# Kernel tuning notes

Hardware: AMD Instinct MI355X
Metric: run time of the kernel (lower is better)

Reference implementation:

```python
import jax, jax.numpy as jnp
import numpy as np

N, D, H1, H2 = 8192, 768, 512, 256


def _nig_head(x, W1, b1, W2, b2, Wh, bh):
    # Linear -> GELU -> (dropout=id) -> Linear -> GELU -> Linear head, then softplus transforms
    h = jax.nn.gelu(x @ W1 + b1, approximate=False)
    h = jax.nn.gelu(h @ W2 + b2, approximate=False)
    r = h @ Wh + bh  # [N, 4]
    mu = r[:, 0]
    v = jax.nn.softplus(r[:, 1]) + 1e-6
    a = jax.nn.softplus(r[:, 2]) + 1.0 + 1e-6
    b = jax.nn.softplus(r[:, 3]) + 1e-6
    return mu, v, a, b


def setup_inputs() -> dict:
    key = jax.random.key(0)
    ks = jax.random.split(key, 16)
    f32 = jnp.float32
    sd = 1.0 / np.sqrt(D)

    def lin(k, din, dout):
        kw, kb = jax.random.split(k)
        W = jax.random.normal(kw, (din, dout), f32) * (1.0 / np.sqrt(din))
        b = jax.random.normal(kb, (dout,), f32) * 0.01
        return W, b

    X = jax.random.normal(ks[0], (N, D), f32)
    Wq = jax.random.normal(ks[1], (D, D), f32) * sd
    Wk = jax.random.normal(ks[2], (D, D), f32) * sd
    Wg, bg = lin(ks[3], D, D)
    gam = jnp.array(1.0, f32)
    ih_W1, ih_b1 = lin(ks[4], D, H1)
    ih_W2, ih_b2 = lin(ks[5], H1, H2)
    ih_Wh, ih_bh = lin(ks[6], H2, 4)
    fh_W1, fh_b1 = lin(ks[7], D, H1)
    fh_W2, fh_b2 = lin(ks[8], H1, H2)
    fh_Wh, fh_bh = lin(ks[9], H2, 4)
    return {
        "X": X, "Wq": Wq, "Wk": Wk, "Wg": Wg, "bg": bg, "gam": gam,
        "ih_W1": ih_W1, "ih_b1": ih_b1, "ih_W2": ih_W2, "ih_b2": ih_b2,
        "ih_Wh": ih_Wh, "ih_bh": ih_bh,
        "fh_W1": fh_W1, "fh_b1": fh_b1, "fh_W2": fh_W2, "fh_b2": fh_b2,
        "fh_Wh": fh_Wh, "fh_bh": fh_bh,
    }


def reference(X, Wq, Wk, Wg, bg, gam,
              ih_W1, ih_b1, ih_W2, ih_b2, ih_Wh, ih_bh,
              fh_W1, fh_b1, fh_W2, fh_b2, fh_Wh, fh_bh):
    # initial NIG head -> epistemic uncertainty -> gate
    m0, v0, a0, b0 = _nig_head(X, ih_W1, ih_b1, ih_W2, ih_b2, ih_Wh, ih_bh)
    u0 = b0 / jnp.maximum(a0 - 1.0, 1e-8)
    G = 1.0 - gam * jax.nn.sigmoid(u0)  # [N]

    # dense attention adjacency
    scale = jnp.sqrt(jnp.asarray(D, X.dtype))
    Q = X @ Wq
    K = X @ Wk
    A = jax.nn.softmax(Q @ K.T / scale, axis=-1)  # [N, N]

    # uncertainty outer-product gate + row renormalization
    A_gated = A * G[None, :] * G[:, None]
    Dinv = 1.0 / jnp.maximum(A_gated.sum(-1, keepdims=True), 1e-8)

    # degree-normalized GCN aggregation + linear + GELU
    M = jax.nn.gelu((A_gated * Dinv) @ X @ Wg + bg, approximate=False)

    # final NIG head on residual
    mu, v, al, be = _nig_head(X + M, fh_W1, fh_b1, fh_W2, fh_b2, fh_Wh, fh_bh)
    return (m0, v0, a0, b0, mu, v, al, be)
```

## Files before the change

kernel.cpp:

```cpp
#include <hip/hip_runtime.h>
#include <hip/hip_bf16.h>
#include <hip/hip_fp8.h>
#include <math.h>
#include <stdint.h>
#include <stddef.h>


#define NT    8192
#define DD    768
#define DH1   512
#define DH2   256
#define SPAN  4096

typedef __attribute__((ext_vector_type(8))) short  short8;
typedef __attribute__((ext_vector_type(4))) float  f32x4;
typedef __attribute__((ext_vector_type(2))) long   longx2;

#define MFMA16(a, b, c) __builtin_amdgcn_mfma_f32_16x16x32_bf16((a), (b), (c), 0, 0, 0)
#define MFMAF8(a, b, c) __builtin_amdgcn_mfma_f32_16x16x32_fp8_fp8((a), (b), (c), 0, 0, 0)

__device__ __forceinline__ float bf2f(__hip_bfloat16 x) { return __bfloat162float(x); }
__device__ __forceinline__ __hip_bfloat16 f2bf(float x) { return __float2bfloat16(x); }
__device__ __forceinline__ uint8_t f2fp8(float x) { return __hip_fp8_e4m3(x).__x; }

__device__ __forceinline__ float gelu_f(float x) {
    return 0.5f * x * (1.0f + erff(x * 0.7071067811865476f));
}
__device__ __forceinline__ float softplus_f(float x) {
    return (x > 20.0f) ? x : log1pf(expf(x));
}

__device__ __forceinline__ void gload16(const void* g, void* l) {
    __builtin_amdgcn_global_load_lds(
        (const __attribute__((address_space(1))) void*)g,
        (__attribute__((address_space(3))) void*)l, 16, 0, 0);
}

template <int N>
__device__ __forceinline__ void wait_barrier() {
    asm volatile("s_waitcnt vmcnt(%0)\n\ts_barrier" :: "i"(N) : "memory");
}
__device__ __forceinline__ void plain_barrier() {
    asm volatile("s_barrier" ::: "memory");
}

__device__ __forceinline__ void xcd_remap(int& bx, int& by) {
    const int nbx = gridDim.x, nby = gridDim.y;
    if ((nby & 7) == 0) {
        const int lin = by * nbx + bx;
        const int x   = lin & 7;
        const int s   = lin >> 3;
        bx = s % nbx;
        by = x + 8 * (s / nbx);
    }
}

template <int EPI, bool SPLIT, int TM, int TN>
__global__ __launch_bounds__(256)
void gemm_bt(const __hip_bfloat16* __restrict__ Ahi, const __hip_bfloat16* __restrict__ Alo, int lda,
             const __hip_bfloat16* __restrict__ Bhi, const __hip_bfloat16* __restrict__ Blo, int ldb,
             __hip_bfloat16* __restrict__ obf_hi, __hip_bfloat16* __restrict__ obf_lo,
             uint8_t* __restrict__ of8, int ldc,
             const float* __restrict__ bias, int K)
{
    constexpr int NB  = SPLIT ? 2 : 1;
    constexpr int WRM = (TM == 128 && TN == 128) ? 2 : (TM == 128 ? 4 : 2);
    constexpr int WCN = 4 / WRM;
    constexpr int WTM = TM / WRM;
    constexpr int WTN = TN / WCN;
    constexpr int MI  = WTM / 16;
    constexpr int NI  = WTN / 16;
    constexpr int PA  = TM / 64;
    constexpr int PB  = TN / 64;
    constexpr int LPI = (PA + PB) * NB;

    __shared__ __align__(16) __hip_bfloat16 As[NB][2][TM * 32];
    __shared__ __align__(16) __hip_bfloat16 Bs[NB][2][TN * 32];

    const int tid  = threadIdx.x;
    const int wave = tid >> 6;
    const int lane = tid & 63;
    int bx = blockIdx.x, by = blockIdx.y;
    xcd_remap(bx, by);
    const int tm = by * TM;
    const int tn = bx * TN;

    const int srow  = tid >> 2;
    const int sgcol = ((tid & 3) ^ ((srow >> 1) & 3)) * 8;
    const int lofs  = srow * 32 + (tid & 3) * 8;

    size_t aoffs[PA], boffs[PB];
#pragma unroll
    for (int p = 0; p < PA; ++p) aoffs[p] = (size_t)(tm + p * 64 + srow) * lda + sgcol;
#pragma unroll
    for (int p = 0; p < PB; ++p) boffs[p] = (size_t)(tn + p * 64 + srow) * ldb + sgcol;

    auto stage = [&](int k0, int buf) {
#pragma unroll
        for (int p = 0; p < PA; ++p)
            gload16(Ahi + aoffs[p] + k0, &As[0][buf][p * 2048 + lofs]);
#pragma unroll
        for (int p = 0; p < PB; ++p)
            gload16(Bhi + boffs[p] + k0, &Bs[0][buf][p * 2048 + lofs]);
        if constexpr (SPLIT) {
#pragma unroll
            for (int p = 0; p < PA; ++p)
                gload16(Alo + aoffs[p] + k0, &As[1][buf][p * 2048 + lofs]);
#pragma unroll
            for (int p = 0; p < PB; ++p)
                gload16(Blo + boffs[p] + k0, &Bs[1][buf][p * 2048 + lofs]);
        }
    };

    f32x4 acc[MI][NI];
#pragma unroll
    for (int i = 0; i < MI; ++i)
#pragma unroll
        for (int j = 0; j < NI; ++j) {
            f32x4 z = {0.0f, 0.0f, 0.0f, 0.0f};
            acc[i][j] = z;
        }

    const int wm   = (wave / WCN) * WTM;
    const int wn   = (wave % WCN) * WTN;
    const int l16  = lane & 15;
    const int quad = lane >> 4;
    const int rchunk = (quad ^ ((l16 >> 1) & 3)) * 8;
    const int arow0  = (wm + l16) * 32 + rchunk;
    const int brow0  = (wn + l16) * 32 + rchunk;

    const int nIter = K >> 5;
    stage(0, 0);
    for (int k = 0; k < nIter; ++k) {
        const int cb = k & 1;
        if (k + 1 < nIter) {
            stage((k + 1) << 5, cb ^ 1);
            wait_barrier<LPI>();
        } else {
            wait_barrier<0>();
        }

        short8 ah[MI], bh[NI];
#pragma unroll
        for (int i = 0; i < MI; ++i) ah[i] = *(const short8*)&As[0][cb][arow0 + i * 512];
#pragma unroll
        for (int j = 0; j < NI; ++j) bh[j] = *(const short8*)&Bs[0][cb][brow0 + j * 512];
        if constexpr (SPLIT) {
            short8 al[MI], bl[NI];
#pragma unroll
            for (int i = 0; i < MI; ++i) al[i] = *(const short8*)&As[1][cb][arow0 + i * 512];
#pragma unroll
            for (int j = 0; j < NI; ++j) bl[j] = *(const short8*)&Bs[1][cb][brow0 + j * 512];
#pragma unroll
            for (int mi = 0; mi < MI; ++mi)
#pragma unroll
                for (int ni = 0; ni < NI; ++ni) {
                    acc[mi][ni] = MFMA16(ah[mi], bh[ni], acc[mi][ni]);
                    acc[mi][ni] = MFMA16(ah[mi], bl[ni], acc[mi][ni]);
                    acc[mi][ni] = MFMA16(al[mi], bh[ni], acc[mi][ni]);
                }
        } else {
#pragma unroll
            for (int mi = 0; mi < MI; ++mi)
#pragma unroll
                for (int ni = 0; ni < NI; ++ni)
                    acc[mi][ni] = MFMA16(ah[mi], bh[ni], acc[mi][ni]);
        }
        plain_barrier();
    }

    const int rbase = tm + wm + quad * 4;
    const int cbase = tn + wn + l16;

    if constexpr (EPI == 0) {
#pragma unroll
        for (int mi = 0; mi < MI; ++mi)
#pragma unroll
            for (int ni = 0; ni < NI; ++ni) {
                f32x4 v = acc[mi][ni];
                const int col = cbase + ni * 16;
#pragma unroll
                for (int r = 0; r < 4; ++r) {
                    size_t idx = (size_t)(rbase + mi * 16 + r) * ldc + col;
                    if (obf_hi) obf_hi[idx] = f2bf(v[r]);
                    if (of8)    of8[idx]    = f2fp8(v[r]);
                }
            }
    } else {
#pragma unroll
        for (int mi = 0; mi < MI; ++mi)
#pragma unroll
            for (int ni = 0; ni < NI; ++ni) {
                f32x4 v = acc[mi][ni];
                const int col = cbase + ni * 16;
                const float b = bias[col];
#pragma unroll
                for (int r = 0; r < 4; ++r) {
                    float g = gelu_f(v[r] + b);
                    __hip_bfloat16 h = f2bf(g);
                    size_t idx = (size_t)(rbase + mi * 16 + r) * ldc + col;
                    obf_hi[idx] = h;
                    if (obf_lo) obf_lo[idx] = f2bf(g - bf2f(h));
                }
            }
    }
}

template <int EPI, int TM, int TN>
__global__ __launch_bounds__(256)
void gemm_f8(const uint8_t* __restrict__ A, int lda,
             const uint8_t* __restrict__ B, int ldb,
             uint8_t* __restrict__ of8, int ldc,
             const float* __restrict__ Gv, float* __restrict__ Esum,
             float* __restrict__ Tsum,
             const float* __restrict__ Xf, const float* __restrict__ bg2,
             const float* __restrict__ Grow, const float* __restrict__ Erow,
             const float* __restrict__ Trow,
             __hip_bfloat16* __restrict__ Yout, int K)
{
    constexpr int WRM = (TM == 128 && TN == 128) ? 2 : (TM == 128 ? 4 : 2);
    constexpr int WCN = 4 / WRM;
    constexpr int WTM = TM / WRM;
    constexpr int WTN = TN / WCN;
    constexpr int MI  = WTM / 16;
    constexpr int NI  = WTN / 16;
    constexpr int PA  = TM / 64;
    constexpr int PB  = TN / 64;
    constexpr int LPI = PA + PB;

    __shared__ __align__(16) uint8_t As[2][TM * 64];
    __shared__ __align__(16) uint8_t Bs[2][TN * 64];

    const int tid  = threadIdx.x;
    const int wave = tid >> 6;
    const int lane = tid & 63;
    int bx = blockIdx.x, by = blockIdx.y;
    xcd_remap(bx, by);
    const int tm = by * TM;
    const int tn = bx * TN;

    const int srow  = tid >> 2;
    const int sgcol = ((tid & 3) ^ ((srow >> 1) & 3)) * 16;
    const int lofs  = tid * 16;

    size_t aoffs[PA], boffs[PB];
#pragma unroll
    for (int p = 0; p < PA; ++p) aoffs[p] = (size_t)(tm + p * 64 + srow) * lda + sgcol;
#pragma unroll
    for (int p = 0; p < PB; ++p) boffs[p] = (size_t)(tn + p * 64 + srow) * ldb + sgcol;

    auto stage = [&](int k0, int buf) {
#pragma unroll
        for (int p = 0; p < PA; ++p)
            gload16(A + aoffs[p] + k0, &As[buf][p * 4096 + lofs]);
#pragma unroll
        for (int p = 0; p < PB; ++p)
            gload16(B + boffs[p] + k0, &Bs[buf][p * 4096 + lofs]);
    };

    f32x4 acc[MI][NI];
#pragma unroll
    for (int i = 0; i < MI; ++i)
#pragma unroll
        for (int j = 0; j < NI; ++j) {
            f32x4 z = {0.0f, 0.0f, 0.0f, 0.0f};
            acc[i][j] = z;
        }

    const int wm   = (wave / WCN) * WTM;
    const int wn   = (wave % WCN) * WTN;
    const int l16  = lane & 15;
    const int quad = lane >> 4;
    const int rchunk = (quad ^ ((l16 >> 1) & 3)) * 16;
    const int arow0  = (wm + l16) * 64 + rchunk;
    const int brow0  = (wn + l16) * 64 + rchunk;

    const int nIter = K >> 6;
    stage(0, 0);
    for (int k = 0; k < nIter; ++k) {
        const int cb = k & 1;
        if (k + 1 < nIter) {
            stage((k + 1) << 6, cb ^ 1);
            wait_barrier<LPI>();
        } else {
            wait_barrier<0>();
        }

        longx2 a[MI], b[NI];
#pragma unroll
        for (int i = 0; i < MI; ++i) a[i] = *(const longx2*)&As[cb][arow0 + i * 1024];
#pragma unroll
        for (int j = 0; j < NI; ++j) b[j] = *(const longx2*)&Bs[cb][brow0 + j * 1024];
#pragma unroll
        for (int mi = 0; mi < MI; ++mi)
#pragma unroll
            for (int ni = 0; ni < NI; ++ni) {
                acc[mi][ni] = MFMAF8(a[mi][0], b[ni][0], acc[mi][ni]);
                acc[mi][ni] = MFMAF8(a[mi][1], b[ni][1], acc[mi][ni]);
            }
        plain_barrier();
    }

    const int rbase = tm + wm + quad * 4;
    const int cbase = tn + wn + l16;

    if constexpr (EPI == 2) {
        const float SCL = 0.03608439182435161f;
#pragma unroll
        for (int mi = 0; mi < MI; ++mi) {
            float sE[4] = {0.f, 0.f, 0.f, 0.f};
            float sT[4] = {0.f, 0.f, 0.f, 0.f};
#pragma unroll
            for (int ni = 0; ni < NI; ++ni) {
                f32x4 v = acc[mi][ni];
                const int col = cbase + ni * 16;
                const float g = Gv[col];
#pragma unroll
                for (int r = 0; r < 4; ++r) {
                    float we = __expf(v[r] * SCL);
                    float w  = we * g;
                    of8[(size_t)(rbase + mi * 16 + r) * ldc + col] = f2fp8(w);
                    sE[r] += we;
                    sT[r] += w;
                }
            }
#pragma unroll
            for (int st = 1; st < 16; st <<= 1)
#pragma unroll
                for (int r = 0; r < 4; ++r) {
                    sE[r] += __shfl_xor(sE[r], st);
                    sT[r] += __shfl_xor(sT[r], st);
                }
            if (l16 == 0) {
#pragma unroll
                for (int r = 0; r < 4; ++r) {
                    atomicAdd(&Esum[rbase + mi * 16 + r], sE[r]);
                    atomicAdd(&Tsum[rbase + mi * 16 + r], sT[r]);
                }
            }
        }
    } else {
#pragma unroll
        for (int mi = 0; mi < MI; ++mi) {
#pragma unroll
            for (int r = 0; r < 4; ++r) {
                const int row = rbase + mi * 16 + r;
                const float g = Grow[row], e = Erow[row], t = Trow[row];
                const float denom = fmaxf(g * t / e, 1e-8f);
                const float alpha = g / (e * denom);
#pragma unroll
                for (int ni = 0; ni < NI; ++ni) {
                    const int col = cbase + ni * 16;
                    const float m = alpha * acc[mi][ni][r];
                    const size_t idx = (size_t)row * ldc + col;
                    Yout[idx] = f2bf(Xf[idx] + gelu_f(m + bg2[col]));
                }
            }
        }
    }
}

__global__ __launch_bounds__(256)
void transpose_f2b(const float* __restrict__ in, int ldin,
                   __hip_bfloat16* __restrict__ ohi, __hip_bfloat16* __restrict__ olo, int ldout)
{
    __shared__ float t[32][33];
    const int tx = threadIdx.x & 31;
    const int ty = threadIdx.x >> 5;
    const int r0 = blockIdx.y * 32;
    const int c0 = blockIdx.x * 32;
#pragma unroll
    for (int j = 0; j < 32; j += 8)
        t[ty + j][tx] = in[(size_t)(r0 + ty + j) * ldin + c0 + tx];
    __syncthreads();
#pragma unroll
    for (int j = 0; j < 32; j += 8) {
        float x = t[tx][ty + j];
        __hip_bfloat16 h = f2bf(x);
        size_t o = (size_t)(c0 + ty + j) * ldout + r0 + tx;
        ohi[o] = h;
        if (olo) olo[o] = f2bf(x - bf2f(h));
    }
}

__global__ __launch_bounds__(256)
void transpose_f8(const uint8_t* __restrict__ in, int ldin,
                  uint8_t* __restrict__ out, int ldout)
{
    __shared__ uint8_t t[32][33];
    const int tx = threadIdx.x & 31;
    const int ty = threadIdx.x >> 5;
    const int r0 = blockIdx.y * 32;
    const int c0 = blockIdx.x * 32;
#pragma unroll
    for (int j = 0; j < 32; j += 8)
        t[ty + j][tx] = in[(size_t)(r0 + ty + j) * ldin + c0 + tx];
    __syncthreads();
#pragma unroll
    for (int j = 0; j < 32; j += 8)
        out[(size_t)(c0 + ty + j) * ldout + r0 + tx] = t[tx][ty + j];
}

__global__ __launch_bounds__(256)
void cvt_split(const float* __restrict__ in, __hip_bfloat16* __restrict__ hi,
               __hip_bfloat16* __restrict__ lo)
{
    const int i = (blockIdx.x * 256 + threadIdx.x) * 4;
    f32x4 v = *(const f32x4*)(in + i);
#pragma unroll
    for (int k = 0; k < 4; ++k) {
        __hip_bfloat16 h = f2bf(v[k]);
        hi[i + k] = h;
        lo[i + k] = f2bf(v[k] - bf2f(h));
    }
}

__global__ __launch_bounds__(256)
void head_tail(const __hip_bfloat16* __restrict__ H2hi, const __hip_bfloat16* __restrict__ H2lo,
               const float* __restrict__ Wh, const float* __restrict__ bh,
               const float* __restrict__ gamp,
               float* __restrict__ outBase, float* __restrict__ Gout)
{
    __shared__ float sa[64], sb[64];
    const int tid = threadIdx.x;
    const int rl  = tid >> 2;
    const int c   = tid & 3;
    const int row = blockIdx.x * 64 + rl;
    const __hip_bfloat16* hh = H2hi + (size_t)row * DH2;
    const __hip_bfloat16* hl = H2lo ? H2lo + (size_t)row * DH2 : nullptr;
    float acc = bh[c];
    if (hl) {
        for (int k = 0; k < DH2; ++k)
            acc = fmaf(bf2f(hh[k]) + bf2f(hl[k]), Wh[k * 4 + c], acc);
    } else {
        for (int k = 0; k < DH2; ++k)
            acc = fmaf(bf2f(hh[k]), Wh[k * 4 + c], acc);
    }
    float sp = softplus_f(acc);
    if (c == 0) {
        outBase[row] = acc;
    } else if (c == 1) {
        outBase[NT + row] = sp + 1e-6f;
    } else if (c == 2) {
        float a0 = (sp + 1.0f) + 1e-6f;
        outBase[2 * NT + row] = a0;
        if (Gout) sa[rl] = a0 - 1.0f;
    } else {
        float b0 = sp + 1e-6f;
        outBase[3 * NT + row] = b0;
        if (Gout) sb[rl] = b0;
    }
    if (Gout != nullptr) {
        __syncthreads();
        if (c == 0) {
            float u   = sb[rl] / fmaxf(sa[rl], 1e-8f);
            float sig = 1.0f / (1.0f + expf(-u));
            Gout[row] = 1.0f - gamp[0] * sig;
        }
    }
}

extern "C" void kernel_launch(void* const* d_in, const int* in_sizes, int n_in,
                              void* d_out, int out_size, void* d_ws, size_t ws_size,
                              hipStream_t stream)
{
    (void)in_sizes; (void)n_in; (void)out_size; (void)ws_size;
    const float* X   = (const float*)d_in[0];
    const float* Wq  = (const float*)d_in[1];
    const float* Wk  = (const float*)d_in[2];
    const float* Wg  = (const float*)d_in[3];
    const float* bg  = (const float*)d_in[4];
    const float* gam = (const float*)d_in[5];
    const float* iW1 = (const float*)d_in[6];
    const float* ib1 = (const float*)d_in[7];
    const float* iW2 = (const float*)d_in[8];
    const float* ib2 = (const float*)d_in[9];
    const float* iWh = (const float*)d_in[10];
    const float* ibh = (const float*)d_in[11];
    const float* fW1 = (const float*)d_in[12];
    const float* fb1 = (const float*)d_in[13];
    const float* fW2 = (const float*)d_in[14];
    const float* fb2 = (const float*)d_in[15];
    const float* fWh = (const float*)d_in[16];
    const float* fbh = (const float*)d_in[17];
    float* out = (float*)d_out;

    char* cur = (char*)d_ws;
    auto alloc = [&](size_t bytes) -> char* {
        char* p = cur;
        cur += (bytes + 255) & ~(size_t)255;
        return p;
    };
    typedef __hip_bfloat16 bf;

    char* regA = alloc((size_t)NT * NT);
    uint8_t* Wp = (uint8_t*)regA;
    bf* Xhi  = (bf*)(regA);
    bf* Xlo  = (bf*)(regA + (size_t)NT * DD * 2);
    bf* H1hi = (bf*)(regA + (size_t)NT * DD * 4);
    bf* H1lo = (bf*)(regA + (size_t)NT * DD * 4 + (size_t)NT * DH1 * 2);
    bf* H2hi = (bf*)(regA + (size_t)NT * DD * 4 + (size_t)NT * DH1 * 4);
    bf* H2lo = (bf*)(regA + (size_t)NT * DD * 4 + (size_t)NT * DH1 * 4 + (size_t)NT * DH2 * 2);

    bf* WqkvT  = (bf*)alloc((size_t)3 * DD * DD * 2);
    bf* iW1hiT = (bf*)alloc((size_t)DH1 * DD * 2);
    bf* iW1loT = (bf*)alloc((size_t)DH1 * DD * 2);
    bf* iW2hiT = (bf*)alloc((size_t)DH2 * DH1 * 2);
    bf* iW2loT = (bf*)alloc((size_t)DH2 * DH1 * 2);
    bf* fW1hiT = (bf*)alloc((size_t)DH1 * DD * 2);
    bf* fW2hiT = (bf*)alloc((size_t)DH2 * DH1 * 2);
    uint8_t* QKVf8 = (uint8_t*)alloc((size_t)NT * 3 * DD);
    uint8_t* VTf8  = (uint8_t*)alloc((size_t)DD * NT);
    float* G    = (float*)alloc((size_t)NT * 4);
    float* E    = (float*)alloc((size_t)NT * 4);
    float* T    = (float*)alloc((size_t)NT * 4);
    bf* Yhi    = (bf*)alloc((size_t)NT * DD * 2);

    const dim3 blk(256);

    cvt_split<<<dim3(NT * DD / 1024), blk, 0, stream>>>(X, Xhi, Xlo);
    transpose_f2b<<<dim3(DD / 32, DD / 32), blk, 0, stream>>>(Wq, DD, WqkvT, nullptr, DD);
    transpose_f2b<<<dim3(DD / 32, DD / 32), blk, 0, stream>>>(Wk, DD, WqkvT + (size_t)DD * DD, nullptr, DD);
    transpose_f2b<<<dim3(DD / 32, DD / 32), blk, 0, stream>>>(Wg, DD, WqkvT + (size_t)2 * DD * DD, nullptr, DD);
    transpose_f2b<<<dim3(DH1 / 32, DD / 32), blk, 0, stream>>>(iW1, DH1, iW1hiT, iW1loT, DD);
    transpose_f2b<<<dim3(DH2 / 32, DH1 / 32), blk, 0, stream>>>(iW2, DH2, iW2hiT, iW2loT, DH1);
    transpose_f2b<<<dim3(DH1 / 32, DD / 32), blk, 0, stream>>>(fW1, DH1, fW1hiT, nullptr, DD);
    transpose_f2b<<<dim3(DH2 / 32, DH1 / 32), blk, 0, stream>>>(fW2, DH2, fW2hiT, nullptr, DH1);

    gemm_bt<1, true, 64, 64><<<dim3(DH1 / 64, NT / 64), blk, 0, stream>>>(
        Xhi, Xlo, DD, iW1hiT, iW1loT, DD, H1hi, H1lo, nullptr, DH1, ib1, DD);
    gemm_bt<1, true, 64, 64><<<dim3(DH2 / 64, NT / 64), blk, 0, stream>>>(
        H1hi, H1lo, DH1, iW2hiT, iW2loT, DH1, H2hi, H2lo, nullptr, DH2, ib2, DH1);
    head_tail<<<dim3(NT / 64), blk, 0, stream>>>(H2hi, H2lo, iWh, ibh, gam, out, G);

    gemm_bt<0, false, 128, 128><<<dim3(3 * DD / 128, NT / 128), blk, 0, stream>>>(
        Xhi, nullptr, DD, WqkvT, nullptr, DD, nullptr, nullptr, QKVf8, 3 * DD,
        nullptr, DD);
    transpose_f8<<<dim3(DD / 32, NT / 32), blk, 0, stream>>>(QKVf8 + 2 * DD, 3 * DD, VTf8, NT);

    hipMemsetAsync(E, 0, (size_t)NT * 4, stream);
    hipMemsetAsync(T, 0, (size_t)NT * 4, stream);

    for (int p = 0; p < 2; ++p) {
        const uint8_t* Kp = QKVf8 + (size_t)p * SPAN * (3 * DD) + DD;
        gemm_f8<2, 128, 128><<<dim3(SPAN / 128, NT / 128), blk, 0, stream>>>(
            QKVf8, 3 * DD, Kp, 3 * DD, Wp + (size_t)p * SPAN, NT,
            G + p * SPAN, E, T, nullptr, nullptr, nullptr, nullptr, nullptr, nullptr, DD);
    }

    gemm_f8<4, 64, 64><<<dim3(DD / 64, NT / 64), blk, 0, stream>>>(
        Wp, NT, VTf8, NT, nullptr, DD,
        nullptr, nullptr, nullptr, X, bg, G, E, T, Yhi, NT);

    gemm_bt<1, false, 64, 64><<<dim3(DH1 / 64, NT / 64), blk, 0, stream>>>(
        Yhi, nullptr, DD, fW1hiT, nullptr, DD, H1hi, nullptr, nullptr, DH1, fb1, DD);
    gemm_bt<1, false, 64, 64><<<dim3(DH2 / 64, NT / 64), blk, 0, stream>>>(
        H1hi, nullptr, DH1, fW2hiT, nullptr, DH1, H2hi, nullptr, nullptr, DH2, fb2, DH1);
    head_tail<<<dim3(NT / 64), blk, 0, stream>>>(H2hi, nullptr, fWh, fbh, gam, out + 4 * NT, nullptr);
}
```

Baseline: 548.6 us.

## Load FP8 GEMM A operand directly into registers, bypassing LDS staging

The A tile is no longer staged through shared memory. Each wave loads its A fragments straight from global memory into registers, double-buffered across an unrolled pair of K iterations, while B still goes through LDS with async loads. This removes LDS traffic and shared-memory footprint for A, which may allow higher occupancy. In exchange, A rows are read redundantly by every wave column (WCN waves), global loads are less coalesced, and the wait count LPI assumes the register loads are counted in the same vmcnt queue.

```diff
diff --git a/kernel.cpp b/kernel.cpp
--- a/kernel.cpp
+++ b/kernel.cpp
@@ -224,11 +224,9 @@
     constexpr int WTN = TN / WCN;
     constexpr int MI  = WTM / 16;
     constexpr int NI  = WTN / 16;
-    constexpr int PA  = TM / 64;
     constexpr int PB  = TN / 64;
-    constexpr int LPI = PA + PB;
-
-    __shared__ __align__(16) uint8_t As[2][TM * 64];
+    constexpr int LPI = PB + MI;
+
     __shared__ __align__(16) uint8_t Bs[2][TN * 64];
 
     const int tid  = threadIdx.x;
@@ -243,16 +241,11 @@
     const int sgcol = ((tid & 3) ^ ((srow >> 1) & 3)) * 16;
     const int lofs  = tid * 16;
 
-    size_t aoffs[PA], boffs[PB];
-#pragma unroll
-    for (int p = 0; p < PA; ++p) aoffs[p] = (size_t)(tm + p * 64 + srow) * lda + sgcol;
+    size_t boffs[PB];
 #pragma unroll
     for (int p = 0; p < PB; ++p) boffs[p] = (size_t)(tn + p * 64 + srow) * ldb + sgcol;
 
-    auto stage = [&](int k0, int buf) {
-#pragma unroll
-        for (int p = 0; p < PA; ++p)
-            gload16(A + aoffs[p] + k0, &As[buf][p * 4096 + lofs]);
+    auto stageB = [&](int k0, int buf) {
 #pragma unroll
         for (int p = 0; p < PB; ++p)
             gload16(B + boffs[p] + k0, &Bs[buf][p * 4096 + lofs]);
@@ -272,33 +265,56 @@
     const int l16  = lane & 15;
     const int quad = lane >> 4;
     const int rchunk = (quad ^ ((l16 >> 1) & 3)) * 16;
-    const int arow0  = (wm + l16) * 64 + rchunk;
     const int brow0  = (wn + l16) * 64 + rchunk;
 
+    const uint8_t* ap[MI];
+#pragma unroll
+    for (int i = 0; i < MI; ++i)
+        ap[i] = A + (size_t)(tm + wm + i * 16 + l16) * lda + quad * 16;
+
+    longx2 a0[MI], a1[MI];
+    auto loadA = [&](longx2* dst, int kIter) {
+#pragma unroll
+        for (int i = 0; i < MI; ++i)
+            dst[i] = *(const longx2*)(ap[i] + (size_t)kIter * 64);
+    };
+    auto compute = [&](const longx2* a, int buf) {
+        longx2 b[NI];
+#pragma unroll
+        for (int j = 0; j < NI; ++j) b[j] = *(const longx2*)&Bs[buf][brow0 + j * 1024];
+#pragma unroll
+        for (int mi = 0; mi < MI; ++mi)
+#pragma unroll
+            for (int ni = 0; ni < NI; ++ni) {
+                acc[mi][ni] = MFMAF8(a[mi][0], b[ni][0], acc[mi][ni]);
+                acc[mi][ni] = MFMAF8(a[mi][1], b[ni][1], acc[mi][ni]);
+            }
+    };
+
     const int nIter = K >> 6;
-    stage(0, 0);
-    for (int k = 0; k < nIter; ++k) {
-        const int cb = k & 1;
+    stageB(0, 0);
+    loadA(a0, 0);
+    for (int k = 0; k < nIter; k += 2) {
         if (k + 1 < nIter) {
-            stage((k + 1) << 6, cb ^ 1);
+            stageB((k + 1) << 6, 1);
+            loadA(a1, k + 1);
             wait_barrier<LPI>();
         } else {
             wait_barrier<0>();
         }
-
-        longx2 a[MI], b[NI];
-#pragma unroll
-        for (int i = 0; i < MI; ++i) a[i] = *(const longx2*)&As[cb][arow0 + i * 1024];
-#pragma unroll
-        for (int j = 0; j < NI; ++j) b[j] = *(const longx2*)&Bs[cb][brow0 + j * 1024];
-#pragma unroll
-        for (int mi = 0; mi < MI; ++mi)
-#pragma unroll
-            for (int ni = 0; ni < NI; ++ni) {
-                acc[mi][ni] = MFMAF8(a[mi][0], b[ni][0], acc[mi][ni]);
-                acc[mi][ni] = MFMAF8(a[mi][1], b[ni][1], acc[mi][ni]);
-            }
+        compute(a0, 0);
         plain_barrier();
+        if (k + 1 < nIter) {
+            if (k + 2 < nIter) {
+                stageB((k + 2) << 6, 0);
+                loadA(a0, k + 2);
+                wait_barrier<LPI>();
+            } else {
+                wait_barrier<0>();
+            }
+            compute(a1, 1);
+            plain_barrier();
+        }
     }
 
     const int rbase = tm + wm + quad * 4;
```

After: 704.2 us. 28.4% more time.
